# Kernel optimization log

Measured on AMD Instinct MI355X. Metric: run time of the kernel, lower is better.

## Reference

```python
import jax, jax.numpy as jnp
import numpy as np

K = 3          # kernel size
STRIDE = 1
PAD = 1
DIL = 1


def setup_inputs() -> dict:
    key = jax.random.key(0)
    k1, k2, k3 = jax.random.split(key, 3)
    N, Cin, H, W = 8, 128, 64, 64
    Cout = 128
    x = jax.random.normal(k1, (N, Cin, H, W), dtype=jnp.float32)
    # offset channels: 2 * deformable_groups * K*K = 18, interleaved (dy, dx) per tap
    offset = jax.random.normal(k2, (N, 2 * K * K, H, W), dtype=jnp.float32)
    weight = jax.random.normal(k3, (Cout, Cin, K, K), dtype=jnp.float32) / np.sqrt(Cin * K * K)
    return {"x": x, "offset": offset, "weight": weight}


def _deform_conv(x, offset, weight):
    N, Cin, H, W = x.shape
    Cout = weight.shape[0]
    KK = K * K
    Ho, Wo = offset.shape[2], offset.shape[3]

    off = offset.reshape(N, KK, 2, Ho, Wo)
    dy = off[:, :, 0]  # [N, KK, Ho, Wo]
    dx = off[:, :, 1]

    kh = jnp.repeat(jnp.arange(K), K).astype(x.dtype)   # [KK]
    kw = jnp.tile(jnp.arange(K), K).astype(x.dtype)     # [KK]
    base_i = (jnp.arange(Ho) * STRIDE - PAD).astype(x.dtype)  # [Ho]
    base_j = (jnp.arange(Wo) * STRIDE - PAD).astype(x.dtype)  # [Wo]

    # Sampling positions: [N, KK, Ho, Wo]
    py = base_i[None, None, :, None] + (kh * DIL)[None, :, None, None] + dy
    px = base_j[None, None, None, :] + (kw * DIL)[None, :, None, None] + dx

    y0 = jnp.floor(py)
    x0 = jnp.floor(px)
    wy1 = py - y0
    wx1 = px - x0
    wy0 = 1.0 - wy1
    wx0 = 1.0 - wx1
    y0i = y0.astype(jnp.int32)
    x0i = x0.astype(jnp.int32)
    y1i = y0i + 1
    x1i = x0i + 1

    x_flat = x.reshape(N, Cin, H * W)

    def gather(yi, xi):
        # zero-padding outside the image
        mask = ((yi >= 0) & (yi < H) & (xi >= 0) & (xi < W)).astype(x.dtype)
        idx = jnp.clip(yi, 0, H - 1) * W + jnp.clip(xi, 0, W - 1)  # [N,KK,Ho,Wo]
        v = jnp.take_along_axis(x_flat, idx.reshape(N, 1, -1), axis=2)  # [N,Cin,KK*Ho*Wo]
        v = v.reshape(N, Cin, KK, Ho, Wo)
        return v * mask[:, None]

    sampled = (gather(y0i, x0i) * (wy0 * wx0)[:, None]
               + gather(y0i, x1i) * (wy0 * wx1)[:, None]
               + gather(y1i, x0i) * (wy1 * wx0)[:, None]
               + gather(y1i, x1i) * (wy1 * wx1)[:, None])  # [N,Cin,KK,Ho,Wo]

    w = weight.reshape(Cout, Cin, KK)
    return jnp.einsum('nckij,ock->noij', sampled, w)


def reference(x, offset, weight):
    return _deform_conv(x, offset, weight)
```

## Files before the change

### kernel.cpp

```cpp
#include <hip/hip_runtime.h>


#define H  64
#define W  64
#define CIN 128
#define COUT 128
#define NB 8
#define KK 9

typedef short bf16x8 __attribute__((ext_vector_type(8)));
typedef float f32x4  __attribute__((ext_vector_type(4)));

__device__ __forceinline__ unsigned short f2bf(float f) {
    unsigned u = __builtin_bit_cast(unsigned, f);
    u += 0x7FFFu + ((u >> 16) & 1u);
    return (unsigned short)(u >> 16);
}
__device__ __forceinline__ float lo_f(unsigned u) { return __builtin_bit_cast(float, u << 16); }
__device__ __forceinline__ float hi_f(unsigned u) { return __builtin_bit_cast(float, u & 0xFFFF0000u); }

__global__ void prep_weight(const float* __restrict__ w, unsigned short* __restrict__ wt) {
    int idx = blockIdx.x * 256 + threadIdx.x;
    if (idx >= KK * COUT * CIN) return;
    int kk = idx / (COUT * CIN);
    int r  = idx - kk * (COUT * CIN);
    int co = r >> 7;
    int c  = r & 127;
    wt[idx] = f2bf(w[(co * CIN + c) * KK + kk]);
}

__global__ void prep_x(const float* __restrict__ x, unsigned short* __restrict__ xt) {
    __shared__ float tile[CIN][W + 1];
    int b = blockIdx.x;
    int n = b >> 6, y = b & 63;
    int t = threadIdx.x;
    int l = t & 63, g = t >> 6;
    const float* src = x + ((size_t)n * CIN * H + y) * W;
    #pragma unroll
    for (int i = 0; i < 32; ++i) {
        int c = g * 32 + i;
        tile[c][l] = src[(size_t)c * H * W + l];
    }
    __syncthreads();
    int xp = t >> 2;
    int cb = (t & 3) * 32;
    unsigned short* dst = xt + (((size_t)(n * H + y) * W + xp) * CIN + cb);
    unsigned rr[16];
    #pragma unroll
    for (int i = 0; i < 16; ++i) {
        float v0 = tile[cb + 2 * i][xp];
        float v1 = tile[cb + 2 * i + 1][xp];
        rr[i] = (unsigned)f2bf(v0) | ((unsigned)f2bf(v1) << 16);
    }
    #pragma unroll
    for (int i = 0; i < 4; ++i)
        ((uint4*)dst)[i] = make_uint4(rr[4*i], rr[4*i+1], rr[4*i+2], rr[4*i+3]);
}

__global__ __launch_bounds__(512, 4) void deform_main(
        const float* __restrict__ offs, const unsigned short* __restrict__ xt,
        const unsigned short* __restrict__ wt, float* __restrict__ out) {
    __shared__ __attribute__((aligned(16))) unsigned short samp[64][CIN + 8];
    __shared__ __attribute__((aligned(16))) unsigned short wts[COUT][CIN + 8];

    int b = blockIdx.x;
    int n = b >> 6, ho = b & 63;
    int t = threadIdx.x;
    int lane = t & 63, wv = t >> 6;
    int lm = lane & 15, lq = lane >> 4;
    int prow = ((wv >> 1) << 4) + lm;
    int cobase = (wv & 1) << 6;

    f32x4 acc[4] = {{0,0,0,0},{0,0,0,0},{0,0,0,0},{0,0,0,0}};

    int p  = t >> 3;
    int cb = (t & 7) << 4;
    const float* offbase = offs + (((size_t)n * 2 * KK) * H + ho) * W + p;

    for (int kk = 0; kk < KK; ++kk) {
        {
            int co = t >> 2;
            int ch = (t & 3) << 5;
            const uint4* src = (const uint4*)(wt + (((size_t)kk * COUT + co) << 7) + ch);
            uint4* dst = (uint4*)&wts[co][ch];
            #pragma unroll
            for (int i = 0; i < 4; ++i) dst[i] = src[i];
        }
        {
            float dy = offbase[(size_t)(2 * kk) * H * W];
            float dx = offbase[(size_t)(2 * kk + 1) * H * W];
            float py = (float)(ho - 1 + kk / 3) + dy;
            float px = (float)(p  - 1 + kk % 3) + dx;
            float y0f = floorf(py), x0f = floorf(px);
            float wy1 = py - y0f, wx1 = px - x0f;
            float wy0 = 1.f - wy1, wx0 = 1.f - wx1;
            int y0 = (int)y0f, x0 = (int)x0f;
            int y1 = y0 + 1, x1 = x0 + 1;
            bool vy0 = (unsigned)y0 < (unsigned)H, vy1 = (unsigned)y1 < (unsigned)H;
            bool vx0 = (unsigned)x0 < (unsigned)W, vx1 = (unsigned)x1 < (unsigned)W;
            float w00 = (vy0 && vx0) ? wy0 * wx0 : 0.f;
            float w01 = (vy0 && vx1) ? wy0 * wx1 : 0.f;
            float w10 = (vy1 && vx0) ? wy1 * wx0 : 0.f;
            float w11 = (vy1 && vx1) ? wy1 * wx1 : 0.f;
            int yc0 = min(max(y0, 0), H - 1), yc1 = min(max(y1, 0), H - 1);
            int xc0 = min(max(x0, 0), W - 1), xc1 = min(max(x1, 0), W - 1);
            const unsigned short* r0 = xt + (size_t)(n * H + yc0) * W * CIN + cb;
            const unsigned short* r1 = xt + (size_t)(n * H + yc1) * W * CIN + cb;
            const unsigned short* b00 = r0 + xc0 * CIN;
            const unsigned short* b01 = r0 + xc1 * CIN;
            const unsigned short* b10 = r1 + xc0 * CIN;
            const unsigned short* b11 = r1 + xc1 * CIN;
            #pragma unroll
            for (int j = 0; j < 2; ++j) {
                uint4 q00 = *(const uint4*)(b00 + 8 * j);
                uint4 q01 = *(const uint4*)(b01 + 8 * j);
                uint4 q10 = *(const uint4*)(b10 + 8 * j);
                uint4 q11 = *(const uint4*)(b11 + 8 * j);
                const unsigned* a0 = (const unsigned*)&q00;
                const unsigned* a1 = (const unsigned*)&q01;
                const unsigned* a2 = (const unsigned*)&q10;
                const unsigned* a3 = (const unsigned*)&q11;
                unsigned rr[4];
                #pragma unroll
                for (int i = 0; i < 4; ++i) {
                    float v0 = w00*lo_f(a0[i]) + w01*lo_f(a1[i]) + w10*lo_f(a2[i]) + w11*lo_f(a3[i]);
                    float v1 = w00*hi_f(a0[i]) + w01*hi_f(a1[i]) + w10*hi_f(a2[i]) + w11*hi_f(a3[i]);
                    rr[i] = (unsigned)f2bf(v0) | ((unsigned)f2bf(v1) << 16);
                }
                *(uint4*)&samp[p][cb + 8 * j] = make_uint4(rr[0], rr[1], rr[2], rr[3]);
            }
        }
        __syncthreads();
        #pragma unroll
        for (int ct = 0; ct < 4; ++ct) {
            bf16x8 a = *(const bf16x8*)&samp[prow][(ct << 5) + (lq << 3)];
            #pragma unroll
            for (int nt = 0; nt < 4; ++nt) {
                bf16x8 bf = *(const bf16x8*)&wts[cobase + (nt << 4) + lm][(ct << 5) + (lq << 3)];
                acc[nt] = __builtin_amdgcn_mfma_f32_16x16x32_bf16(a, bf, acc[nt], 0, 0, 0);
            }
        }
        __syncthreads();
    }
    int wo = ((wv >> 1) << 4) + (lq << 2);
    #pragma unroll
    for (int nt = 0; nt < 4; ++nt) {
        int co = cobase + (nt << 4) + lm;
        *(f32x4*)(out + (((size_t)(n * COUT + co) * H + ho) * W + wo)) = acc[nt];
    }
}

extern "C" void kernel_launch(void* const* d_in, const int* in_sizes, int n_in,
                              void* d_out, int out_size, void* d_ws, size_t ws_size,
                              hipStream_t stream) {
    const float* x      = (const float*)d_in[0];
    const float* offset = (const float*)d_in[1];
    const float* weight = (const float*)d_in[2];
    float* out = (float*)d_out;

    unsigned short* xt = (unsigned short*)d_ws;
    unsigned short* wt = (unsigned short*)((char*)d_ws + (size_t)NB*H*W*CIN*2);

    hipLaunchKernelGGL(prep_weight, dim3((KK*COUT*CIN + 255) / 256), dim3(256), 0, stream,
                       weight, wt);
    hipLaunchKernelGGL(prep_x, dim3(NB * H), dim3(256), 0, stream, x, xt);
    hipLaunchKernelGGL(deform_main, dim3(NB * H), dim3(512), 0, stream,
                       offset, xt, wt, out);
}
```

Baseline: 112.7 us.

## Fuse prep kernels, load weights directly to registers, double-buffer sample tile

The two preprocessing kernels become one launch, with extra blocks handling the weight conversion. The x transpose now uses float4 loads and a rotated shared-memory layout to cut bank conflicts. In the main kernel the weight tile is no longer staged through shared memory: each wave loads its MFMA B operands straight from global memory into registers, split around the sampling work. The sample buffer is double-buffered so the second barrier per tap can go, at the cost of more registers and shared memory.

```diff
diff --git a/kernel.cpp b/kernel.cpp
--- a/kernel.cpp
+++ b/kernel.cpp
@@ -19,37 +19,42 @@
 __device__ __forceinline__ float lo_f(unsigned u) { return __builtin_bit_cast(float, u << 16); }
 __device__ __forceinline__ float hi_f(unsigned u) { return __builtin_bit_cast(float, u & 0xFFFF0000u); }
 
-__global__ void prep_weight(const float* __restrict__ w, unsigned short* __restrict__ wt) {
-    int idx = blockIdx.x * 256 + threadIdx.x;
-    if (idx >= KK * COUT * CIN) return;
-    int kk = idx / (COUT * CIN);
-    int r  = idx - kk * (COUT * CIN);
-    int co = r >> 7;
-    int c  = r & 127;
-    wt[idx] = f2bf(w[(co * CIN + c) * KK + kk]);
-}
-
-__global__ void prep_x(const float* __restrict__ x, unsigned short* __restrict__ xt) {
-    __shared__ float tile[CIN][W + 1];
+__global__ void prep_all(const float* __restrict__ x, const float* __restrict__ w,
+                         unsigned short* __restrict__ xt, unsigned short* __restrict__ wt) {
     int b = blockIdx.x;
+    int t = threadIdx.x;
+    if (b >= NB * H) {
+        int idx = (b - NB * H) * 256 + t;
+        if (idx < KK * COUT * CIN) {
+            int kk = idx / (COUT * CIN);
+            int r  = idx - kk * (COUT * CIN);
+            int co = r >> 7;
+            int c  = r & 127;
+            wt[idx] = f2bf(w[(co * CIN + c) * KK + kk]);
+        }
+        return;
+    }
+    __shared__ float tile[CIN][W + 4];
     int n = b >> 6, y = b & 63;
-    int t = threadIdx.x;
-    int l = t & 63, g = t >> 6;
     const float* src = x + ((size_t)n * CIN * H + y) * W;
     #pragma unroll
-    for (int i = 0; i < 32; ++i) {
-        int c = g * 32 + i;
-        tile[c][l] = src[(size_t)c * H * W + l];
+    for (int it = 0; it < 8; ++it) {
+        int idx = it * 256 + t;
+        int c  = idx >> 4;
+        int x4 = (idx & 15) << 2;
+        int xs = (x4 + ((c >> 5) << 4)) & 63;
+        *(float4*)&tile[c][xs] = *(const float4*)(src + (size_t)c * H * W + x4);
     }
     __syncthreads();
     int xp = t >> 2;
-    int cb = (t & 3) * 32;
-    unsigned short* dst = xt + (((size_t)(n * H + y) * W + xp) * CIN + cb);
+    int cbch = (t & 3) << 5;
+    int xr = (xp + ((cbch >> 5) << 4)) & 63;
+    unsigned short* dst = xt + (((size_t)(n * H + y) * W + xp) * CIN + cbch);
     unsigned rr[16];
     #pragma unroll
     for (int i = 0; i < 16; ++i) {
-        float v0 = tile[cb + 2 * i][xp];
-        float v1 = tile[cb + 2 * i + 1][xp];
+        float v0 = tile[cbch + 2 * i][xr];
+        float v1 = tile[cbch + 2 * i + 1][xr];
         rr[i] = (unsigned)f2bf(v0) | ((unsigned)f2bf(v1) << 16);
     }
     #pragma unroll
@@ -60,8 +65,7 @@
 __global__ __launch_bounds__(512, 4) void deform_main(
         const float* __restrict__ offs, const unsigned short* __restrict__ xt,
         const unsigned short* __restrict__ wt, float* __restrict__ out) {
-    __shared__ __attribute__((aligned(16))) unsigned short samp[64][CIN + 8];
-    __shared__ __attribute__((aligned(16))) unsigned short wts[COUT][CIN + 8];
+    __shared__ __attribute__((aligned(16))) unsigned short samp[2][64][CIN + 8];
 
     int b = blockIdx.x;
     int n = b >> 6, ho = b & 63;
@@ -76,16 +80,18 @@
     int p  = t >> 3;
     int cb = (t & 7) << 4;
     const float* offbase = offs + (((size_t)n * 2 * KK) * H + ho) * W + p;
+    const unsigned short* xrow = xt + (size_t)n * H * W * CIN + cb;
+    const unsigned short* wfb = wt + (((size_t)(cobase + lm)) << 7) + (lq << 3);
 
     for (int kk = 0; kk < KK; ++kk) {
-        {
-            int co = t >> 2;
-            int ch = (t & 3) << 5;
-            const uint4* src = (const uint4*)(wt + (((size_t)kk * COUT + co) << 7) + ch);
-            uint4* dst = (uint4*)&wts[co][ch];
+        const unsigned short* wk = wfb + ((size_t)kk << 14);
+        bf16x8 b01[2][4], b23[2][4];
+        #pragma unroll
+        for (int ct = 0; ct < 2; ++ct)
             #pragma unroll
-            for (int i = 0; i < 4; ++i) dst[i] = src[i];
-        }
+            for (int nt = 0; nt < 4; ++nt)
+                b01[ct][nt] = *(const bf16x8*)(wk + (nt << 11) + (ct << 5));
+
         {
             float dy = offbase[(size_t)(2 * kk) * H * W];
             float dx = offbase[(size_t)(2 * kk + 1) * H * W];
@@ -104,18 +110,18 @@
             float w11 = (vy1 && vx1) ? wy1 * wx1 : 0.f;
             int yc0 = min(max(y0, 0), H - 1), yc1 = min(max(y1, 0), H - 1);
             int xc0 = min(max(x0, 0), W - 1), xc1 = min(max(x1, 0), W - 1);
-            const unsigned short* r0 = xt + (size_t)(n * H + yc0) * W * CIN + cb;
-            const unsigned short* r1 = xt + (size_t)(n * H + yc1) * W * CIN + cb;
-            const unsigned short* b00 = r0 + xc0 * CIN;
-            const unsigned short* b01 = r0 + xc1 * CIN;
-            const unsigned short* b10 = r1 + xc0 * CIN;
-            const unsigned short* b11 = r1 + xc1 * CIN;
+            const unsigned short* r0 = xrow + (size_t)yc0 * W * CIN;
+            const unsigned short* r1 = xrow + (size_t)yc1 * W * CIN;
+            const unsigned short* c00 = r0 + xc0 * CIN;
+            const unsigned short* c01 = r0 + xc1 * CIN;
+            const unsigned short* c10 = r1 + xc0 * CIN;
+            const unsigned short* c11 = r1 + xc1 * CIN;
             #pragma unroll
             for (int j = 0; j < 2; ++j) {
-                uint4 q00 = *(const uint4*)(b00 + 8 * j);
-                uint4 q01 = *(const uint4*)(b01 + 8 * j);
-                uint4 q10 = *(const uint4*)(b10 + 8 * j);
-                uint4 q11 = *(const uint4*)(b11 + 8 * j);
+                uint4 q00 = *(const uint4*)(c00 + 8 * j);
+                uint4 q01 = *(const uint4*)(c01 + 8 * j);
+                uint4 q10 = *(const uint4*)(c10 + 8 * j);
+                uint4 q11 = *(const uint4*)(c11 + 8 * j);
                 const unsigned* a0 = (const unsigned*)&q00;
                 const unsigned* a1 = (const unsigned*)&q01;
                 const unsigned* a2 = (const unsigned*)&q10;
@@ -127,20 +133,29 @@
                     float v1 = w00*hi_f(a0[i]) + w01*hi_f(a1[i]) + w10*hi_f(a2[i]) + w11*hi_f(a3[i]);
                     rr[i] = (unsigned)f2bf(v0) | ((unsigned)f2bf(v1) << 16);
                 }
-                *(uint4*)&samp[p][cb + 8 * j] = make_uint4(rr[0], rr[1], rr[2], rr[3]);
+                *(uint4*)&samp[kk & 1][p][cb + 8 * j] = make_uint4(rr[0], rr[1], rr[2], rr[3]);
             }
         }
+        #pragma unroll
+        for (int ct = 0; ct < 2; ++ct)
+            #pragma unroll
+            for (int nt = 0; nt < 4; ++nt)
+                b23[ct][nt] = *(const bf16x8*)(wk + (nt << 11) + ((ct + 2) << 5));
+
         __syncthreads();
+
         #pragma unroll
         for (int ct = 0; ct < 4; ++ct) {
-            bf16x8 a = *(const bf16x8*)&samp[prow][(ct << 5) + (lq << 3)];
+            bf16x8 a = *(const bf16x8*)&samp[kk & 1][prow][(ct << 5) + (lq << 3)];
             #pragma unroll
             for (int nt = 0; nt < 4; ++nt) {
-                bf16x8 bf = *(const bf16x8*)&wts[cobase + (nt << 4) + lm][(ct << 5) + (lq << 3)];
-                acc[nt] = __builtin_amdgcn_mfma_f32_16x16x32_bf16(a, bf, acc[nt], 0, 0, 0);
+                bf16x8 bq = (ct == 0) ? b01[0][nt]
+                          : (ct == 1) ? b01[1][nt]
+                          : (ct == 2) ? b23[0][nt]
+                          :             b23[1][nt];
+                acc[nt] = __builtin_amdgcn_mfma_f32_16x16x32_bf16(a, bq, acc[nt], 0, 0, 0);
             }
         }
-        __syncthreads();
     }
     int wo = ((wv >> 1) << 4) + (lq << 2);
     #pragma unroll
@@ -161,9 +176,9 @@
     unsigned short* xt = (unsigned short*)d_ws;
     unsigned short* wt = (unsigned short*)((char*)d_ws + (size_t)NB*H*W*CIN*2);
 
-    hipLaunchKernelGGL(prep_weight, dim3((KK*COUT*CIN + 255) / 256), dim3(256), 0, stream,
-                       weight, wt);
-    hipLaunchKernelGGL(prep_x, dim3(NB * H), dim3(256), 0, stream, x, xt);
+    int wblocks = (KK * COUT * CIN + 255) / 256;
+    hipLaunchKernelGGL(prep_all, dim3(NB * H + wblocks), dim3(256), 0, stream,
+                       x, weight, xt, wt);
     hipLaunchKernelGGL(deform_main, dim3(NB * H), dim3(512), 0, stream,
                        offset, xt, wt, out);
 }
```

New measurement: 157.1 us. 39.4% more time.
